# Optimization experiments

Measured on AMD Instinct MI355X. Metric: run time of the kernel, lower is better.

Reference implementation:

```python
import jax, jax.numpy as jnp
import numpy as np

B, T, C = 4, 2048, 1024
H, D = 16, 64
EPS = 1.1920929e-07  # torch.finfo(float32).eps, used by F.rms_norm default


def setup_inputs() -> dict:
    key = jax.random.key(0)
    ks = jax.random.split(key, 6)
    x = jax.random.normal(ks[0], (B, T, C), dtype=jnp.float32)
    # rotary cache: theta = 10000^(-2i/D), broadcastable [1, T, 1, D//2]
    inv_freq = 1.0 / (10000.0 ** (jnp.arange(0, D // 2, dtype=jnp.float32) * 2.0 / D))
    ang = jnp.arange(T, dtype=jnp.float32)[:, None] * inv_freq[None, :]  # [T, D//2]
    cos = jnp.cos(ang)[None, :, None, :]
    sin = jnp.sin(ang)[None, :, None, :]
    s = 0.02
    Wq = jax.random.normal(ks[1], (C, C), dtype=jnp.float32) * s
    Wk = jax.random.normal(ks[2], (C, C), dtype=jnp.float32) * s
    Wv = jax.random.normal(ks[3], (C, C), dtype=jnp.float32) * s
    Wo = jax.random.normal(ks[4], (C, C), dtype=jnp.float32) * s
    return {"x": x, "cos": cos, "sin": sin, "Wq": Wq, "Wk": Wk, "Wv": Wv, "Wo": Wo}


def _rope(x, cos, sin):
    d = x.shape[-1] // 2
    x1, x2 = x[..., :d], x[..., d:]
    return jnp.concatenate([x1 * cos + x2 * sin, -x1 * sin + x2 * cos], axis=-1)


def _rmsnorm(x):
    ms = jnp.mean(jnp.square(x), axis=-1, keepdims=True)
    return x * jax.lax.rsqrt(ms + EPS)


def reference(x, cos, sin, Wq, Wk, Wv, Wo):
    Bx, Tx, Cx = x.shape
    q = (x @ Wq.T).reshape(Bx, Tx, H, D)
    k = (x @ Wk.T).reshape(Bx, Tx, H, D)
    v = (x @ Wv.T).reshape(Bx, Tx, H, D)
    q = _rmsnorm(_rope(q, cos, sin))
    k = _rmsnorm(_rope(k, cos, sin))
    scale = 1.0 / jnp.sqrt(jnp.float32(D))
    # non-causal SDPA
    scores = jnp.einsum('bthd,bshd->bhts', q, k) * scale  # [B,H,T,T]
    attn = jax.nn.softmax(scores, axis=-1)
    y = jnp.einsum('bhts,bshd->bthd', attn, v).reshape(Bx, Tx, Cx)
    return y @ Wo.T
```

## Files before the change

kernel.cpp:

```cpp
#include <hip/hip_runtime.h>

#define B_ 4
#define T_ 2048
#define C_ 1024
#define H_ 16
#define D_ 64
#define EPS_ 1.1920929e-07f
#define LOG2E_ 1.4426950408889634f

typedef __attribute__((ext_vector_type(8))) short bf16x8;
typedef __attribute__((ext_vector_type(4))) float f32x4;
typedef __attribute__((ext_vector_type(16))) float f32x16;
typedef unsigned short u16;
typedef unsigned int u32;
typedef __attribute__((ext_vector_type(4))) u32 u32x4;

__device__ inline u16 f2bf(float f) {
  unsigned u = __float_as_uint(f);
  unsigned r = (u + 0x7fffu + ((u >> 16) & 1u)) >> 16;
  return (u16)r;
}

__device__ __forceinline__ void gload16(const void* g, void* l) {
  __builtin_amdgcn_global_load_lds(
      (__attribute__((address_space(1))) void*)g,
      (__attribute__((address_space(3))) void*)l, 16, 0, 0);
}

__global__ __launch_bounds__(256) void cvt_all(const float* __restrict__ x,
                                               const float* __restrict__ wq,
                                               const float* __restrict__ wk,
                                               const float* __restrict__ wv,
                                               const float* __restrict__ wo,
                                               u16* __restrict__ xb,
                                               u16* __restrict__ wqkv,
                                               u16* __restrict__ wob) {
  const int NXB = (int)((size_t)B_ * T_ * C_ / 1024);
  const int WB = (C_ * C_) / 1024;
  const int bid = blockIdx.x;
  const float* src;
  u16* dst;
  int i;
  if (bid < NXB) {
    src = x; dst = xb; i = bid * 1024 + threadIdx.x * 4;
  } else {
    const int wb = bid - NXB;
    const int t = wb / WB;
    const int r = wb - t * WB;
    src = (t == 0) ? wq : (t == 1) ? wk : (t == 2) ? wv : wo;
    dst = (t == 3) ? wob : (wqkv + (size_t)t * (C_ * C_));
    i = r * 1024 + threadIdx.x * 4;
  }
  float4 v = *(const float4*)&src[i];
  ushort4 o;
  o.x = f2bf(v.x); o.y = f2bf(v.y); o.z = f2bf(v.z); o.w = f2bf(v.w);
  *(ushort4*)&dst[i] = o;
}

__global__ __launch_bounds__(256) void gemm_qkv(const u16* __restrict__ X,
                                                const u16* __restrict__ W,
                                                u16* __restrict__ qb,
                                                u16* __restrict__ kb,
                                                u16* __restrict__ vtb,
                                                const float* __restrict__ cs,
                                                const float* __restrict__ sn,
                                                int M, int K) {
  __shared__ short As[128 * 64];
  __shared__ short Bs[128 * 64];
  const int tid = threadIdx.x;
  const int lane = tid & 63;
  const int w = tid >> 6;
  const int wr = w >> 1, wc = w & 1;
  const int hwlin = blockIdx.x + 24 * blockIdx.y;
  const int lg = (hwlin & 7) * 192 + (hwlin >> 3);
  const int bx = lg % 24, by = lg / 24;
  const int m0 = by * 128, n0 = bx * 128;
  const int lrow = lane >> 3;
  const int lcol = (lane & 7) * 8;

  f32x4 acc[4][4];
#pragma unroll
  for (int mi = 0; mi < 4; ++mi)
#pragma unroll
    for (int ni = 0; ni < 4; ++ni)
      acc[mi][ni] = (f32x4){0.f, 0.f, 0.f, 0.f};

  const int r = lane & 15;
  const int quad = lane >> 4;

  for (int kt = 0; kt < K; kt += 64) {
#pragma unroll
    for (int i = 0; i < 4; ++i) {
      const int row = w * 32 + i * 8;
      gload16(&X[(size_t)(m0 + row + lrow) * K + kt + lcol], &As[row * 64]);
      gload16(&W[(size_t)(n0 + row + lrow) * K + kt + lcol], &Bs[row * 64]);
    }
    __syncthreads();
#pragma unroll
    for (int kc = 0; kc < 2; ++kc) {
      const int ko = kc * 32 + quad * 8;
      bf16x8 a[4], b[4];
#pragma unroll
      for (int mi = 0; mi < 4; ++mi)
        a[mi] = *(const bf16x8*)&As[(wr * 64 + mi * 16 + r) * 64 + ko];
#pragma unroll
      for (int ni = 0; ni < 4; ++ni)
        b[ni] = *(const bf16x8*)&Bs[(wc * 64 + ni * 16 + r) * 64 + ko];
#pragma unroll
      for (int mi = 0; mi < 4; ++mi)
#pragma unroll
        for (int ni = 0; ni < 4; ++ni)
          acc[mi][ni] = __builtin_amdgcn_mfma_f32_16x16x32_bf16(a[mi], b[ni], acc[mi][ni], 0, 0, 0);
    }
    __syncthreads();
  }

  const int which = bx >> 3;
  const int c0 = (bx & 7) * 128 + wc * 64;

  if (which < 2) {
    u16* dst = (which == 0) ? qb : kb;
#pragma unroll
    for (int mi = 0; mi < 4; ++mi)
#pragma unroll
      for (int j = 0; j < 4; ++j) {
        const int gr = m0 + wr * 64 + mi * 16 + quad * 4 + j;
        const int t = gr & (T_ - 1);
        float o[4];
#pragma unroll
        for (int ni = 0; ni < 2; ++ni) {
          const float c = cs[t * 32 + ni * 16 + r];
          const float s = sn[t * 32 + ni * 16 + r];
          const float x1 = acc[mi][ni][j], x2 = acc[mi][ni + 2][j];
          o[ni]     = x1 * c + x2 * s;
          o[ni + 2] = x2 * c - x1 * s;
        }
        float sq = o[0] * o[0] + o[1] * o[1] + o[2] * o[2] + o[3] * o[3];
        sq += __shfl_xor(sq, 1, 64);
        sq += __shfl_xor(sq, 2, 64);
        sq += __shfl_xor(sq, 4, 64);
        sq += __shfl_xor(sq, 8, 64);
        float rn = rsqrtf(sq * (1.0f / 64.0f) + EPS_);
        if (which == 0) rn *= 0.125f * LOG2E_;
#pragma unroll
        for (int ni = 0; ni < 4; ++ni)
          dst[(size_t)gr * C_ + c0 + ni * 16 + r] = f2bf(o[ni] * rn);
      }
  } else {
    const int h = (bx & 7) * 2 + wc;
    const int gr0 = m0 + wr * 64;
    const int bb = gr0 >> 11;
    const int tbase = gr0 & (T_ - 1);
#pragma unroll
    for (int ni = 0; ni < 4; ++ni) {
      const int d = ni * 16 + r;
      u16* rowp = &vtb[((size_t)((bb * H_ + h) * D_ + d)) * T_ + tbase];
#pragma unroll
      for (int mi = 0; mi < 4; ++mi) {
        u32 lo, hi2;
        asm("v_cvt_pk_bf16_f32 %0, %1, %2" : "=v"(lo) : "v"(acc[mi][ni][0]), "v"(acc[mi][ni][1]));
        asm("v_cvt_pk_bf16_f32 %0, %1, %2" : "=v"(hi2) : "v"(acc[mi][ni][2]), "v"(acc[mi][ni][3]));
        u16* p = rowp + mi * 16 + quad * 2;
        *(u32*)&p[0] = lo;
        *(u32*)&p[8] = hi2;
      }
    }
  }
}

__global__ __launch_bounds__(256) void gemm_out(const u16* __restrict__ X,
                                                const u16* __restrict__ W,
                                                float* __restrict__ Y,
                                                int M, int N, int K) {
  __shared__ short As[128 * 64];
  __shared__ short Bs[128 * 64];
  const int tid = threadIdx.x;
  const int lane = tid & 63;
  const int w = tid >> 6;
  const int wr = w >> 1, wc = w & 1;
  const int hwlin = blockIdx.x + 8 * blockIdx.y;
  const int lg = (hwlin & 7) * 64 + (hwlin >> 3);
  const int bx = lg & 7, by = lg >> 3;
  const int m0 = by * 128, n0 = bx * 128;
  const int lrow = lane >> 3;
  const int lcol = (lane & 7) * 8;

  f32x4 acc[4][4];
#pragma unroll
  for (int mi = 0; mi < 4; ++mi)
#pragma unroll
    for (int ni = 0; ni < 4; ++ni)
      acc[mi][ni] = (f32x4){0.f, 0.f, 0.f, 0.f};

  const int r = lane & 15;
  const int quad = lane >> 4;

  for (int kt = 0; kt < K; kt += 64) {
#pragma unroll
    for (int i = 0; i < 4; ++i) {
      const int row = w * 32 + i * 8;
      gload16(&X[(size_t)(m0 + row + lrow) * K + kt + lcol], &As[row * 64]);
      gload16(&W[(size_t)(n0 + row + lrow) * K + kt + lcol], &Bs[row * 64]);
    }
    __syncthreads();
#pragma unroll
    for (int kc = 0; kc < 2; ++kc) {
      const int ko = kc * 32 + quad * 8;
      bf16x8 a[4], b[4];
#pragma unroll
      for (int mi = 0; mi < 4; ++mi)
        a[mi] = *(const bf16x8*)&As[(wr * 64 + mi * 16 + r) * 64 + ko];
#pragma unroll
      for (int ni = 0; ni < 4; ++ni)
        b[ni] = *(const bf16x8*)&Bs[(wc * 64 + ni * 16 + r) * 64 + ko];
#pragma unroll
      for (int mi = 0; mi < 4; ++mi)
#pragma unroll
        for (int ni = 0; ni < 4; ++ni)
          acc[mi][ni] = __builtin_amdgcn_mfma_f32_16x16x32_bf16(a[mi], b[ni], acc[mi][ni], 0, 0, 0);
    }
    __syncthreads();
  }

#pragma unroll
  for (int mi = 0; mi < 4; ++mi)
#pragma unroll
    for (int ni = 0; ni < 4; ++ni) {
      const int gc = n0 + wc * 64 + ni * 16 + r;
#pragma unroll
      for (int j = 0; j < 4; ++j) {
        const int gr = m0 + wr * 64 + mi * 16 + quad * 4 + j;
        Y[(size_t)gr * N + gc] = acc[mi][ni][j];
      }
    }
}

__global__ __launch_bounds__(256) void flash_mfma(const u16* __restrict__ Qb,
                                                  const u16* __restrict__ Kb,
                                                  const u16* __restrict__ Vtb,
                                                  u16* __restrict__ Yb) {
  __shared__ u16 Ks[2][64][72];
  __shared__ u16 Vt[2][64][72];
  const int tid = threadIdx.x;
  const int lane = tid & 63;
  const int w = tid >> 6;
  const int c = lane & 31;
  const int hi = lane >> 5;
  const int bh = blockIdx.x, qt = blockIdx.y;
  const int b = bh >> 4, h = bh & 15;
  const int srow = lane;
  const int sd0 = w * 16;
  const int vrow = tid >> 2;
  const int vco = (tid & 3) * 16;

  const u16* kbase = Kb + ((size_t)(b * T_ + srow) * H_ + h) * D_ + sd0;
  const u16* vbase = Vtb + ((size_t)(bh * 64 + vrow)) * T_ + vco;
  const int KSTRIDE = 64 * H_ * D_;

  bf16x8 k0, k1, v0, v1;
  k0 = *(const bf16x8*)&kbase[0];
  k1 = *(const bf16x8*)&kbase[8];
  v0 = *(const bf16x8*)&vbase[0];
  v1 = *(const bf16x8*)&vbase[8];

  {
    const int row = tid >> 1, half = tid & 1;
    const size_t g = ((size_t)((b * T_ + qt * 128 + row) * H_ + h)) * D_ + half * 32;
    u16* qd = (row < 64) ? &Ks[0][row][half * 32] : &Ks[1][row - 64][half * 32];
    *(bf16x8*)&qd[0]  = *(const bf16x8*)&Qb[g];
    *(bf16x8*)&qd[8]  = *(const bf16x8*)&Qb[g + 8];
    *(bf16x8*)&qd[16] = *(const bf16x8*)&Qb[g + 16];
    *(bf16x8*)&qd[24] = *(const bf16x8*)&Qb[g + 24];
  }
  __syncthreads();
  bf16x8 qf[4];
  {
    const int qr = w * 32 + c;
    const u16* qs = (qr < 64) ? &Ks[0][qr][0] : &Ks[1][qr - 64][0];
#pragma unroll
    for (int ks = 0; ks < 4; ++ks)
      qf[ks] = *(const bf16x8*)&qs[ks * 16 + hi * 8];
  }
  __syncthreads();

  *(bf16x8*)&Ks[0][srow][sd0] = k0;
  *(bf16x8*)&Ks[0][srow][sd0 + 8] = k1;
  *(bf16x8*)&Vt[0][vrow][vco] = v0;
  *(bf16x8*)&Vt[0][vrow][vco + 8] = v1;
  k0 = *(const bf16x8*)&kbase[KSTRIDE];
  k1 = *(const bf16x8*)&kbase[KSTRIDE + 8];
  v0 = *(const bf16x8*)&vbase[64];
  v1 = *(const bf16x8*)&vbase[64 + 8];
  __syncthreads();

  f32x16 oacc[2], oacc_l;
  oacc[0] = (f32x16)(0.f);
  oacc[1] = (f32x16)(0.f);
  oacc_l  = (f32x16)(0.f);
  bf16x8 onesv;
#pragma unroll
  for (int i = 0; i < 8; ++i) onesv[i] = (short)0x3F80;

  const int NT = T_ / 64;
#pragma unroll 2
  for (int t = 0; t < NT; ++t) {
    const int cur = t & 1;

    f32x16 s0 = (f32x16)(0.f), s1 = (f32x16)(0.f);
    __builtin_amdgcn_s_setprio(1);
#pragma unroll
    for (int ks = 0; ks < 4; ++ks) {
      bf16x8 kf0 = *(const bf16x8*)&Ks[cur][c][ks * 16 + hi * 8];
      bf16x8 kf1 = *(const bf16x8*)&Ks[cur][32 + c][ks * 16 + hi * 8];
      s0 = __builtin_amdgcn_mfma_f32_32x32x16_bf16(kf0, qf[ks], s0, 0, 0, 0);
      s1 = __builtin_amdgcn_mfma_f32_32x32x16_bf16(kf1, qf[ks], s1, 0, 0, 0);
    }
    __builtin_amdgcn_s_setprio(0);

    if (t + 1 < NT) {
      const int nxt = cur ^ 1;
      *(bf16x8*)&Ks[nxt][srow][sd0] = k0;
      *(bf16x8*)&Ks[nxt][srow][sd0 + 8] = k1;
      *(bf16x8*)&Vt[nxt][vrow][vco] = v0;
      *(bf16x8*)&Vt[nxt][vrow][vco + 8] = v1;
      if (t + 2 < NT) {
        const int gk = (t + 2) * KSTRIDE;
        k0 = *(const bf16x8*)&kbase[gk];
        k1 = *(const bf16x8*)&kbase[gk + 8];
        const int gv = (t + 2) * 64;
        v0 = *(const bf16x8*)&vbase[gv];
        v1 = *(const bf16x8*)&vbase[gv + 8];
      }
    }

    u32 wrd[2][4][2];
#pragma unroll
    for (int m = 0; m < 4; ++m)
#pragma unroll
      for (int p = 0; p < 2; ++p) {
        float a0 = __builtin_amdgcn_exp2f(s0[m * 4 + p * 2]);
        float a1 = __builtin_amdgcn_exp2f(s0[m * 4 + p * 2 + 1]);
        float b0 = __builtin_amdgcn_exp2f(s1[m * 4 + p * 2]);
        float b1 = __builtin_amdgcn_exp2f(s1[m * 4 + p * 2 + 1]);
        asm("v_cvt_pk_bf16_f32 %0, %1, %2" : "=v"(wrd[0][m][p]) : "v"(a0), "v"(a1));
        asm("v_cvt_pk_bf16_f32 %0, %1, %2" : "=v"(wrd[1][m][p]) : "v"(b0), "v"(b1));
      }
#pragma unroll
    for (int kt2 = 0; kt2 < 2; ++kt2)
#pragma unroll
      for (int m = 0; m < 4; ++m)
        asm("v_permlane32_swap_b32 %0, %1" : "+v"(wrd[kt2][m][0]), "+v"(wrd[kt2][m][1]));

    bf16x8 pa[4];
    pa[0] = __builtin_bit_cast(bf16x8, (u32x4){wrd[0][0][0], wrd[0][0][1], wrd[0][1][0], wrd[0][1][1]});
    pa[1] = __builtin_bit_cast(bf16x8, (u32x4){wrd[0][2][0], wrd[0][2][1], wrd[0][3][0], wrd[0][3][1]});
    pa[2] = __builtin_bit_cast(bf16x8, (u32x4){wrd[1][0][0], wrd[1][0][1], wrd[1][1][0], wrd[1][1][1]});
    pa[3] = __builtin_bit_cast(bf16x8, (u32x4){wrd[1][2][0], wrd[1][2][1], wrd[1][3][0], wrd[1][3][1]});

    __builtin_amdgcn_s_setprio(1);
#pragma unroll
    for (int ks = 0; ks < 4; ++ks) {
      bf16x8 vf0 = *(const bf16x8*)&Vt[cur][c][ks * 16 + hi * 8];
      bf16x8 vf1 = *(const bf16x8*)&Vt[cur][32 + c][ks * 16 + hi * 8];
      oacc[0] = __builtin_amdgcn_mfma_f32_32x32x16_bf16(pa[ks], vf0, oacc[0], 0, 0, 0);
      oacc[1] = __builtin_amdgcn_mfma_f32_32x32x16_bf16(pa[ks], vf1, oacc[1], 0, 0, 0);
      oacc_l  = __builtin_amdgcn_mfma_f32_32x32x16_bf16(pa[ks], onesv, oacc_l, 0, 0, 0);
    }
    __builtin_amdgcn_s_setprio(0);
    __syncthreads();
  }

#pragma unroll
  for (int v = 0; v < 16; ++v) {
    const float inv = 1.0f / oacc_l[v];
    const int q = (v & 3) + 8 * (v >> 2) + 4 * hi;
    const int tq = qt * 128 + w * 32 + q;
    const size_t gbase = ((size_t)((b * T_ + tq) * H_ + h)) * D_;
    Yb[gbase + c]      = f2bf(oacc[0][v] * inv);
    Yb[gbase + 32 + c] = f2bf(oacc[1][v] * inv);
  }
}

extern "C" void kernel_launch(void* const* d_in, const int* in_sizes, int n_in,
                              void* d_out, int out_size, void* d_ws, size_t ws_size,
                              hipStream_t stream) {
  const float* x    = (const float*)d_in[0];
  const float* cosb = (const float*)d_in[1];
  const float* sinb = (const float*)d_in[2];
  const float* Wq   = (const float*)d_in[3];
  const float* Wk   = (const float*)d_in[4];
  const float* Wv   = (const float*)d_in[5];
  const float* Wo   = (const float*)d_in[6];
  float* out = (float*)d_out;

  const size_t NE = (size_t)B_ * T_ * C_;
  const int CC = C_ * C_;
  u16* xb   = (u16*)d_ws;
  u16* qb   = xb + NE;
  u16* kb   = qb + NE;
  u16* vtb  = kb + NE;
  u16* wqkv = vtb + NE;
  u16* wob  = wqkv + 3 * (size_t)CC;
  u16* yb   = xb;

  const int M = B_ * T_;

  const int NXB = (int)(NE / 1024);
  const int NWB = 4 * (CC / 1024);
  cvt_all<<<NXB + NWB, 256, 0, stream>>>(x, Wq, Wk, Wv, Wo, xb, wqkv, wob);

  dim3 qg(24, M / 128), gb(256);
  gemm_qkv<<<qg, gb, 0, stream>>>(xb, wqkv, qb, kb, vtb, cosb, sinb, M, C_);

  dim3 fg(B_ * H_, T_ / 128);
  flash_mfma<<<fg, 256, 0, stream>>>(qb, kb, vtb, yb);

  dim3 og(C_ / 128, M / 128);
  gemm_out<<<og, gb, 0, stream>>>(yb, wob, out, M, C_, C_);
}
```

Measured before the change: 311.1 us.

## Double-buffer LDS and widen GEMM tiles to 128x256 with 8 waves

```diff
diff --git a/kernel.cpp b/kernel.cpp
--- a/kernel.cpp
+++ b/kernel.cpp
@@ -57,7 +57,7 @@
   *(ushort4*)&dst[i] = o;
 }
 
-__global__ __launch_bounds__(256) void gemm_qkv(const u16* __restrict__ X,
+__global__ __launch_bounds__(512) void gemm_qkv(const u16* __restrict__ X,
                                                 const u16* __restrict__ W,
                                                 u16* __restrict__ qb,
                                                 u16* __restrict__ kb,
@@ -65,16 +65,15 @@
                                                 const float* __restrict__ cs,
                                                 const float* __restrict__ sn,
                                                 int M, int K) {
-  __shared__ short As[128 * 64];
-  __shared__ short Bs[128 * 64];
+  __shared__ short As[2][128 * 64];
+  __shared__ short Bs[2][256 * 64];
   const int tid = threadIdx.x;
   const int lane = tid & 63;
-  const int w = tid >> 6;
-  const int wr = w >> 1, wc = w & 1;
-  const int hwlin = blockIdx.x + 24 * blockIdx.y;
-  const int lg = (hwlin & 7) * 192 + (hwlin >> 3);
-  const int bx = lg % 24, by = lg / 24;
-  const int m0 = by * 128, n0 = bx * 128;
+  const int wid = tid >> 6;
+  const int wm = wid >> 2, wn = wid & 3;
+  const int bx = blockIdx.x, by = blockIdx.y;
+  const int m0 = by * 128, n0 = bx * 256;
+  const int w8 = wid * 8;
   const int lrow = lane >> 3;
   const int lcol = (lane & 7) * 8;
 
@@ -88,24 +87,37 @@
   const int r = lane & 15;
   const int quad = lane >> 4;
 
-  for (int kt = 0; kt < K; kt += 64) {
-#pragma unroll
-    for (int i = 0; i < 4; ++i) {
-      const int row = w * 32 + i * 8;
-      gload16(&X[(size_t)(m0 + row + lrow) * K + kt + lcol], &As[row * 64]);
-      gload16(&W[(size_t)(n0 + row + lrow) * K + kt + lcol], &Bs[row * 64]);
-    }
-    __syncthreads();
+#pragma unroll
+  for (int ra = 0; ra < 2; ++ra)
+    gload16(&X[(size_t)(m0 + ra * 64 + w8 + lrow) * K + lcol], &As[0][(ra * 64 + w8) * 64]);
+#pragma unroll
+  for (int rb = 0; rb < 4; ++rb)
+    gload16(&W[(size_t)(n0 + rb * 64 + w8 + lrow) * K + lcol], &Bs[0][(rb * 64 + w8) * 64]);
+  __syncthreads();
+
+#pragma unroll 2
+  for (int it = 0; it < 16; ++it) {
+    const int cur = it & 1;
+    const int kt = it * 64;
+    if (it + 1 < 16) {
+      const int nb = cur ^ 1;
+#pragma unroll
+      for (int ra = 0; ra < 2; ++ra)
+        gload16(&X[(size_t)(m0 + ra * 64 + w8 + lrow) * K + kt + 64 + lcol], &As[nb][(ra * 64 + w8) * 64]);
+#pragma unroll
+      for (int rb = 0; rb < 4; ++rb)
+        gload16(&W[(size_t)(n0 + rb * 64 + w8 + lrow) * K + kt + 64 + lcol], &Bs[nb][(rb * 64 + w8) * 64]);
+    }
 #pragma unroll
     for (int kc = 0; kc < 2; ++kc) {
       const int ko = kc * 32 + quad * 8;
       bf16x8 a[4], b[4];
 #pragma unroll
       for (int mi = 0; mi < 4; ++mi)
-        a[mi] = *(const bf16x8*)&As[(wr * 64 + mi * 16 + r) * 64 + ko];
+        a[mi] = *(const bf16x8*)&As[cur][(wm * 64 + mi * 16 + r) * 64 + ko];
 #pragma unroll
       for (int ni = 0; ni < 4; ++ni)
-        b[ni] = *(const bf16x8*)&Bs[(wc * 64 + ni * 16 + r) * 64 + ko];
+        b[ni] = *(const bf16x8*)&Bs[cur][(wn * 64 + ni * 16 + r) * 64 + ko];
 #pragma unroll
       for (int mi = 0; mi < 4; ++mi)
 #pragma unroll
@@ -115,8 +127,8 @@
     __syncthreads();
   }
 
-  const int which = bx >> 3;
-  const int c0 = (bx & 7) * 128 + wc * 64;
+  const int which = bx >> 2;
+  const int c0 = (bx & 3) * 256 + wn * 64;
 
   if (which < 2) {
     u16* dst = (which == 0) ? qb : kb;
@@ -124,7 +136,7 @@
     for (int mi = 0; mi < 4; ++mi)
 #pragma unroll
       for (int j = 0; j < 4; ++j) {
-        const int gr = m0 + wr * 64 + mi * 16 + quad * 4 + j;
+        const int gr = m0 + wm * 64 + mi * 16 + quad * 4 + j;
         const int t = gr & (T_ - 1);
         float o[4];
 #pragma unroll
@@ -147,8 +159,8 @@
           dst[(size_t)gr * C_ + c0 + ni * 16 + r] = f2bf(o[ni] * rn);
       }
   } else {
-    const int h = (bx & 7) * 2 + wc;
-    const int gr0 = m0 + wr * 64;
+    const int h = (bx & 3) * 4 + wn;
+    const int gr0 = m0 + wm * 64;
     const int bb = gr0 >> 11;
     const int tbase = gr0 & (T_ - 1);
 #pragma unroll
@@ -168,20 +180,18 @@
   }
 }
 
-__global__ __launch_bounds__(256) void gemm_out(const u16* __restrict__ X,
+__global__ __launch_bounds__(512) void gemm_out(const u16* __restrict__ X,
                                                 const u16* __restrict__ W,
                                                 float* __restrict__ Y,
                                                 int M, int N, int K) {
-  __shared__ short As[128 * 64];
-  __shared__ short Bs[128 * 64];
+  __shared__ short As[2][128 * 64];
+  __shared__ short Bs[2][256 * 64];
   const int tid = threadIdx.x;
   const int lane = tid & 63;
-  const int w = tid >> 6;
-  const int wr = w >> 1, wc = w & 1;
-  const int hwlin = blockIdx.x + 8 * blockIdx.y;
-  const int lg = (hwlin & 7) * 64 + (hwlin >> 3);
-  const int bx = lg & 7, by = lg >> 3;
-  const int m0 = by * 128, n0 = bx * 128;
+  const int wid = tid >> 6;
+  const int wm = wid >> 2, wn = wid & 3;
+  const int m0 = blockIdx.y * 128, n0 = blockIdx.x * 256;
+  const int w8 = wid * 8;
   const int lrow = lane >> 3;
   const int lcol = (lane & 7) * 8;
 
@@ -195,24 +205,37 @@
   const int r = lane & 15;
   const int quad = lane >> 4;
 
-  for (int kt = 0; kt < K; kt += 64) {
-#pragma unroll
-    for (int i = 0; i < 4; ++i) {
-      const int row = w * 32 + i * 8;
-      gload16(&X[(size_t)(m0 + row + lrow) * K + kt + lcol], &As[row * 64]);
-      gload16(&W[(size_t)(n0 + row + lrow) * K + kt + lcol], &Bs[row * 64]);
-    }
-    __syncthreads();
+#pragma unroll
+  for (int ra = 0; ra < 2; ++ra)
+    gload16(&X[(size_t)(m0 + ra * 64 + w8 + lrow) * K + lcol], &As[0][(ra * 64 + w8) * 64]);
+#pragma unroll
+  for (int rb = 0; rb < 4; ++rb)
+    gload16(&W[(size_t)(n0 + rb * 64 + w8 + lrow) * K + lcol], &Bs[0][(rb * 64 + w8) * 64]);
+  __syncthreads();
+
+#pragma unroll 2
+  for (int it = 0; it < 16; ++it) {
+    const int cur = it & 1;
+    const int kt = it * 64;
+    if (it + 1 < 16) {
+      const int nb = cur ^ 1;
+#pragma unroll
+      for (int ra = 0; ra < 2; ++ra)
+        gload16(&X[(size_t)(m0 + ra * 64 + w8 + lrow) * K + kt + 64 + lcol], &As[nb][(ra * 64 + w8) * 64]);
+#pragma unroll
+      for (int rb = 0; rb < 4; ++rb)
+        gload16(&W[(size_t)(n0 + rb * 64 + w8 + lrow) * K + kt + 64 + lcol], &Bs[nb][(rb * 64 + w8) * 64]);
+    }
 #pragma unroll
     for (int kc = 0; kc < 2; ++kc) {
       const int ko = kc * 32 + quad * 8;
       bf16x8 a[4], b[4];
 #pragma unroll
       for (int mi = 0; mi < 4; ++mi)
-        a[mi] = *(const bf16x8*)&As[(wr * 64 + mi * 16 + r) * 64 + ko];
+        a[mi] = *(const bf16x8*)&As[cur][(wm * 64 + mi * 16 + r) * 64 + ko];
 #pragma unroll
       for (int ni = 0; ni < 4; ++ni)
-        b[ni] = *(const bf16x8*)&Bs[(wc * 64 + ni * 16 + r) * 64 + ko];
+        b[ni] = *(const bf16x8*)&Bs[cur][(wn * 64 + ni * 16 + r) * 64 + ko];
 #pragma unroll
       for (int mi = 0; mi < 4; ++mi)
 #pragma unroll
@@ -226,10 +249,10 @@
   for (int mi = 0; mi < 4; ++mi)
 #pragma unroll
     for (int ni = 0; ni < 4; ++ni) {
-      const int gc = n0 + wc * 64 + ni * 16 + r;
+      const int gc = n0 + wn * 64 + ni * 16 + r;
 #pragma unroll
       for (int j = 0; j < 4; ++j) {
-        const int gr = m0 + wr * 64 + mi * 16 + quad * 4 + j;
+        const int gr = m0 + wm * 64 + mi * 16 + quad * 4 + j;
         Y[(size_t)gr * N + gc] = acc[mi][ni][j];
       }
     }
@@ -409,12 +432,12 @@
   const int NWB = 4 * (CC / 1024);
   cvt_all<<<NXB + NWB, 256, 0, stream>>>(x, Wq, Wk, Wv, Wo, xb, wqkv, wob);
 
-  dim3 qg(24, M / 128), gb(256);
+  dim3 qg(12, M / 128), gb(512);
   gemm_qkv<<<qg, gb, 0, stream>>>(xb, wqkv, qb, kb, vtb, cosb, sinb, M, C_);
 
   dim3 fg(B_ * H_, T_ / 128);
   flash_mfma<<<fg, 256, 0, stream>>>(qb, kb, vtb, yb);
 
-  dim3 og(C_ / 128, M / 128);
+  dim3 og(C_ / 256, M / 128);
   gemm_out<<<og, gb, 0, stream>>>(yb, wob, out, M, C_, C_);
 }
```

Result: no change. 309.0 us (-0.7%).
